# Optimization experiments

Measured on AMD Instinct MI355X. Metric: run time of the kernel, lower is better.

The kernel has to match this reference:

```python
import math
import jax, jax.numpy as jnp
import numpy as np

K = 64            # multiplicity per irrep
NE = 10           # num_elements
N_NODES = 10000
N_EDGES = 100000
AVG_NEIGH = 10.0
EDGE_DIM = 8
LS = [0, 1, 2]    # node/intermediate irreps 64x0e+64x1o+64x2e
LS_OUT = [0, 1]   # output irreps 64x0e+64x1o
INV_SQRT_K = 1.0 / math.sqrt(K)
MIX_NORM = 1.0 / math.sqrt(K * NE)

# ---- real spherical-harmonic Clebsch-Gordan coefficients (small l, exact) ----
def _cg(j1, m1, j2, m2, j3, m3):
    if m1 + m2 != m3 or not (abs(j1 - j2) <= j3 <= j1 + j2):
        return 0.0
    f = math.factorial
    pre = math.sqrt((2 * j3 + 1) * f(j1 + j2 - j3) * f(j1 - j2 + j3) * f(-j1 + j2 + j3) / f(j1 + j2 + j3 + 1))
    pre *= math.sqrt(f(j1 + m1) * f(j1 - m1) * f(j2 + m2) * f(j2 - m2) * f(j3 + m3) * f(j3 - m3))
    s = 0.0
    for k in range(j1 + j2 + j3 + 1):
        d = (j1 + j2 - j3 - k, j1 - m1 - k, j2 + m2 - k, j3 - j2 + m1 + k, j3 - j1 - m2 + k)
        if min(d) < 0:
            continue
        s += (-1) ** k / (f(k) * f(d[0]) * f(d[1]) * f(d[2]) * f(d[3]) * f(d[4]))
    return pre * s

def _u_real(l):
    # complex->real SH change of basis: Y_real = U @ Y_complex
    U = np.zeros((2 * l + 1, 2 * l + 1), dtype=np.complex128)
    U[l, l] = 1.0
    s = 1.0 / math.sqrt(2.0)
    for m in range(1, l + 1):
        U[l + m, l + m] = (-1) ** m * s
        U[l + m, l - m] = s
        U[l - m, l + m] = -1j * (-1) ** m * s
        U[l - m, l - m] = 1j * s
    return U

def real_cg(l1, l2, l3):
    C = np.zeros((2 * l1 + 1, 2 * l2 + 1, 2 * l3 + 1), dtype=np.complex128)
    for m1 in range(-l1, l1 + 1):
        for m2 in range(-l2, l2 + 1):
            m3 = m1 + m2
            if abs(m3) <= l3:
                C[l1 + m1, l2 + m2, l3 + m3] = _cg(l1, m1, l2, m2, l3, m3)
    U1, U2, U3 = _u_real(l1), _u_real(l2), _u_real(l3)
    Cr = np.einsum('ai,bj,ck,ijk->abc', U1, U2, U3.conj(), C)
    return np.ascontiguousarray(Cr.real).astype(np.float32)  # real since l1+l2+l3 even

# parity/triangle allowed paths (l1: edge sph, l2: node in, l3: intermediate) -> 11 paths
EDGE_PATHS = [(l1, l2, l3) for l1 in LS for l2 in LS for l3 in LS
              if abs(l1 - l2) <= l3 <= l1 + l2 and (l1 + l2 + l3) % 2 == 0]
N_EDGE_PATHS = len(EDGE_PATHS)  # 11
DEG2_PATHS = [(0, 0, 0), (1, 1, 0), (2, 2, 0), (0, 1, 1), (1, 2, 1)]
DEG3_PATHS = [(0, 0, 0), (1, 1, 0), (0, 1, 1), (1, 0, 1), (1, 2, 1)]
CG_EDGE = [real_cg(*p) for p in EDGE_PATHS]
CG_D2 = [real_cg(*p) for p in DEG2_PATHS]
CG_D3 = [real_cg(*p) for p in DEG3_PATHS]

def split_irreps(x, ls, mul):
    # ir_mul layout: per irrep a [(2l+1)*mul] flat segment, m index outer
    out, o = [], 0
    for l in ls:
        d = (2 * l + 1) * mul
        out.append(x[:, o:o + d].reshape(x.shape[0], 2 * l + 1, mul))
        o += d
    return out


def setup_inputs() -> dict:
    key = jax.random.key(0)
    ks = jax.random.split(key, 20)
    sender = jax.random.randint(ks[0], (N_EDGES,), 0, N_NODES)
    receiver = jax.random.randint(ks[1], (N_EDGES,), 0, N_NODES)
    indices = jax.random.randint(ks[2], (N_NODES,), 0, NE)
    node_attrs = jax.nn.one_hot(indices, NE, dtype=jnp.float32)
    node_feature_in = jax.random.normal(ks[3], (N_NODES, K * 9), dtype=jnp.float32)
    edge_length_embed = jax.random.normal(ks[4], (N_EDGES, EDGE_DIM), dtype=jnp.float32)
    edge_sph_embed = jax.random.normal(ks[5], (N_EDGES, 9), dtype=jnp.float32)
    W_lin_in = jax.random.normal(ks[6], (3, K, K), dtype=jnp.float32)
    mlp_W0 = jax.random.normal(ks[7], (EDGE_DIM, 32), dtype=jnp.float32) / math.sqrt(EDGE_DIM)
    mlp_b0 = jnp.zeros((32,), jnp.float32)
    mlp_W1 = jax.random.normal(ks[8], (32, 32), dtype=jnp.float32) / math.sqrt(32.0)
    mlp_b1 = jnp.zeros((32,), jnp.float32)
    mlp_W2 = jax.random.normal(ks[9], (32, 32), dtype=jnp.float32) / math.sqrt(32.0)
    mlp_b2 = jnp.zeros((32,), jnp.float32)
    mlp_W3 = jax.random.normal(ks[10], (32, N_EDGE_PATHS * K), dtype=jnp.float32) / math.sqrt(32.0)
    mlp_b3 = jnp.zeros((N_EDGE_PATHS * K,), jnp.float32)
    W_mix = jax.random.normal(ks[11], (3, NE, K, K), dtype=jnp.float32)
    w1 = jax.random.normal(ks[12], (NE, 2, K), dtype=jnp.float32)
    w2 = 0.1 * jax.random.normal(ks[13], (NE, len(DEG2_PATHS), K), dtype=jnp.float32)
    w3 = 0.05 * jax.random.normal(ks[14], (NE, len(DEG3_PATHS), K), dtype=jnp.float32)
    W_out_m = jax.random.normal(ks[15], (2, K, K), dtype=jnp.float32)
    W_out_h = jax.random.normal(ks[16], (2, K, K), dtype=jnp.float32)
    return dict(sender=sender, receiver=receiver, indices=indices, node_attrs=node_attrs,
                node_feature_in=node_feature_in, edge_length_embed=edge_length_embed,
                edge_sph_embed=edge_sph_embed, W_lin_in=W_lin_in,
                mlp_W0=mlp_W0, mlp_b0=mlp_b0, mlp_W1=mlp_W1, mlp_b1=mlp_b1,
                mlp_W2=mlp_W2, mlp_b2=mlp_b2, mlp_W3=mlp_W3, mlp_b3=mlp_b3,
                W_mix=W_mix, w1=w1, w2=w2, w3=w3, W_out_m=W_out_m, W_out_h=W_out_h)


def reference(sender, receiver, indices, node_attrs, node_feature_in,
              edge_length_embed, edge_sph_embed, W_lin_in,
              mlp_W0, mlp_b0, mlp_W1, mlp_b1, mlp_W2, mlp_b2, mlp_W3, mlp_b3,
              W_mix, w1, w2, w3, W_out_m, W_out_h):
    N = node_feature_in.shape[0]
    h1 = split_irreps(node_feature_in, LS, K)  # per-l [N, 2l+1, K]
    # ELinear_h1_2_h1p: per-irrep channel mixing
    h1p = [jnp.einsum('nmc,cd->nmd', h1[l], W_lin_in[l]) * INV_SQRT_K for l in LS]
    # residual radial MLP -> per-edge TP path weights [E, P, K]
    h = jax.nn.silu(edge_length_embed @ mlp_W0 + mlp_b0)
    h = h + jax.nn.silu(h @ mlp_W1 + mlp_b1)
    h = h + jax.nn.silu(h @ mlp_W2 + mlp_b2)
    Rl = (h @ mlp_W3 + mlp_b3).reshape(-1, N_EDGE_PATHS, K)
    sph = split_irreps(edge_sph_embed, LS, 1)  # per-l [E, 2l+1, 1]
    gx = [h1p[l][sender] for l in LS]          # gather sender node features
    # channelwise equivariant tensor product with per-edge radial weights
    msg = [None, None, None]
    for p, (l1, l2, l3) in enumerate(EDGE_PATHS):
        t = jnp.einsum('abd,ea,ebc->edc', jnp.asarray(CG_EDGE[p]), sph[l1][:, :, 0], gx[l2])
        t = t * Rl[:, p, None, :]
        msg[l3] = t if msg[l3] is None else msg[l3] + t
    # scatter-sum messages to receivers, normalized by avg num neighbors
    A = [jax.ops.segment_sum(msg[l], receiver, num_segments=N) / AVG_NEIGH for l in LS]
    # element-conditioned mixing (FCTP with num_elements x 0e attrs)
    Amix = [jnp.einsum('nmc,ne,ecd->nmd', A[l], node_attrs, W_mix[l]) * MIX_NORM for l in LS]
    # symmetric contraction (body order 3) with element-dependent channelwise weights
    w1n, w2n, w3n = w1[indices], w2[indices], w3[indices]
    T2 = [jnp.zeros_like(Amix[L]) for L in LS_OUT]
    for p, (l1, l2, L) in enumerate(DEG2_PATHS):
        t = jnp.einsum('abd,nac,nbc->ndc', jnp.asarray(CG_D2[p]), Amix[l1], Amix[l2])
        T2[L] = T2[L] + w2n[:, p, None, :] * t
    T3 = [jnp.zeros_like(Amix[L]) for L in LS_OUT]
    for q, (Lp, l3, L) in enumerate(DEG3_PATHS):
        t = jnp.einsum('abd,nac,nbc->ndc', jnp.asarray(CG_D3[q]), T2[Lp], Amix[l3])
        T3[L] = T3[L] + w3n[:, q, None, :] * t
    B = [w1n[:, L, None, :] * Amix[L] + T2[L] + T3[L] for L in LS_OUT]
    # node_feature_out = ELinear_h1_2_h2(h1) + ELinear_m2_2_h2(B)
    out = []
    for L in LS_OUT:
        y = jnp.einsum('nmc,cd->nmd', h1[L], W_out_h[L]) * INV_SQRT_K
        y = y + jnp.einsum('nmc,cd->nmd', B[L], W_out_m[L]) * INV_SQRT_K
        out.append(y.reshape(N, -1))
    return jnp.concatenate(out, axis=1)  # [N, 4K] = [N, 256]
```

## Files before the change

### kernel.cpp

```cpp
#include <hip/hip_runtime.h>
#include <math.h>

#define NNODES 10000
#define NEDGES 100000
#define EPW 8

struct Cplx { double re, im; };

constexpr double cfact(int n){ double r=1.0; for(int i=2;i<=n;++i) r*=i; return r; }

constexpr double csqrt_(double x){
  if (x<=0.0) return 0.0;
  double g = x<1.0 ? 1.0 : x;
  for (int it=0; it<64; ++it){ double ng = 0.5*(g + x/g); if (ng==g) break; g = ng; }
  return g;
}

constexpr double cg_coeff(int j1,int m1,int j2,int m2,int j3,int m3){
  if (m1+m2!=m3) return 0.0;
  int lo = j1>j2 ? j1-j2 : j2-j1;
  if (j3<lo || j3>j1+j2) return 0.0;
  if (m1<-j1||m1>j1||m2<-j2||m2>j2||m3<-j3||m3>j3) return 0.0;
  double pre = csqrt_((2.0*j3+1.0)*cfact(j1+j2-j3)*cfact(j1-j2+j3)*cfact(-j1+j2+j3)/cfact(j1+j2+j3+1));
  pre *= csqrt_(cfact(j1+m1)*cfact(j1-m1)*cfact(j2+m2)*cfact(j2-m2)*cfact(j3+m3)*cfact(j3-m3));
  double s = 0.0;
  for (int k=0;k<=j1+j2+j3;++k){
    int d0=j1+j2-j3-k, d1=j1-m1-k, d2=j2+m2-k, d3=j3-j2+m1+k, d4=j3-j1-m2+k;
    if (d0<0||d1<0||d2<0||d3<0||d4<0) continue;
    double term = 1.0/(cfact(k)*cfact(d0)*cfact(d1)*cfact(d2)*cfact(d3)*cfact(d4));
    s += (k&1) ? -term : term;
  }
  return pre*s;
}

constexpr Cplx uent(int l,int a,int i){
  const double s = 0.70710678118654752440;
  int ma = a - l;
  if (ma==0) { if (i==l) return Cplx{1.0,0.0}; return Cplx{0.0,0.0}; }
  if (ma>0){
    int m = ma; double sg = (m&1) ? -1.0 : 1.0;
    if (i==l+m) return Cplx{sg*s, 0.0};
    if (i==l-m) return Cplx{s, 0.0};
    return Cplx{0.0,0.0};
  }
  int m = -ma; double sg = (m&1) ? -1.0 : 1.0;
  if (i==l+m) return Cplx{0.0, -sg*s};
  if (i==l-m) return Cplx{0.0, s};
  return Cplx{0.0,0.0};
}

constexpr double real_cg_entry(int l1,int l2,int l3,int a,int b,int c){
  double acc = 0.0;
  int ii0 = a, ii1 = 2*l1-a;
  int jj0 = b, jj1 = 2*l2-b;
  for (int x=0;x<2;++x){
    int i = (x==0)? ii0 : ii1;
    if (x==1 && ii1==ii0) break;
    Cplx u1 = uent(l1,a,i); if (u1.re==0.0 && u1.im==0.0) continue;
    for (int y=0;y<2;++y){
      int j = (y==0)? jj0 : jj1;
      if (y==1 && jj1==jj0) break;
      Cplx u2 = uent(l2,b,j); if (u2.re==0.0 && u2.im==0.0) continue;
      int k = (i-l1)+(j-l2)+l3;
      if (k<0 || k>2*l3) continue;
      Cplx u3 = uent(l3,c,k); if (u3.re==0.0 && u3.im==0.0) continue;
      double cg = cg_coeff(l1,i-l1,l2,j-l2,l3,k-l3);
      if (cg==0.0) continue;
      double pr = u1.re*u2.re - u1.im*u2.im;
      double pi = u1.re*u2.im + u1.im*u2.re;
      acc += (pr*u3.re + pi*u3.im) * cg;
    }
  }
  return acc;
}

struct CGT { float v[5][5][5]; };
constexpr CGT make_cg(int l1,int l2,int l3){
  CGT t{};
  for (int a=0;a<2*l1+1;++a)
    for (int b=0;b<2*l2+1;++b)
      for (int c=0;c<2*l3+1;++c)
        t.v[a][b][c] = (float)real_cg_entry(l1,l2,l3,a,b,c);
  return t;
}

__device__ __forceinline__ float rdlane(float v, int l){
  return __int_as_float(__builtin_amdgcn_readlane(__float_as_int(v), l));
}
__device__ __forceinline__ float silu_(float x){ return x / (1.0f + __expf(-x)); }

template<int L1,int L2,int L3>
__device__ __forceinline__ void tp_accum(const float* sp, const float* g, float rl, float* msg){
  constexpr CGT T = make_cg(L1,L2,L3);
  constexpr int NA = 2*L1+1, NB = 2*L2+1, ND = 2*L3+1;
  float t[ND];
#pragma unroll
  for (int d=0; d<ND; ++d) t[d] = 0.f;
#pragma unroll
  for (int b=0;b<NB;++b){
#pragma unroll
    for (int d=0; d<ND; ++d){
      float u = 0.f; bool any = false;
#pragma unroll
      for (int a=0;a<NA;++a){
        const float cg = T.v[a][b][d];
        if (cg != 0.f){ u = fmaf(cg, sp[a], u); any = true; }
      }
      if (any) t[d] = fmaf(u, g[b], t[d]);
    }
  }
#pragma unroll
  for (int d=0;d<ND;++d) msg[d] = fmaf(rl, t[d], msg[d]);
}

template<int L1,int L2,int L3>
__device__ __forceinline__ void sc_accum(const float* X, const float* Y, float w, float* out){
  constexpr CGT T = make_cg(L1,L2,L3);
  constexpr int NA = 2*L1+1, NB = 2*L2+1, ND = 2*L3+1;
#pragma unroll
  for (int d=0;d<ND;++d){
    float s = 0.f;
#pragma unroll
    for (int a=0;a<NA;++a){
#pragma unroll
      for (int b=0;b<NB;++b){
        const float cg = T.v[a][b][d];
        if (cg != 0.f) s = fmaf(cg*X[a], Y[b], s);
      }
    }
    out[d] = fmaf(w, s, out[d]);
  }
}

__global__ void __launch_bounds__(64) k_lin_in(const float* __restrict__ h1,
                                               const float* __restrict__ W,
                                               float* __restrict__ h1p){
  const int n = blockIdx.x;
  const int d = threadIdx.x;
  const float* row = h1 + (long)n*576;
  float acc[9];
#pragma unroll
  for (int i=0;i<9;++i) acc[i] = 0.f;
  for (int c=0;c<64;++c){
    const float w0 = W[c*64 + d];
    const float w1 = W[4096 + c*64 + d];
    const float w2 = W[8192 + c*64 + d];
    acc[0] = fmaf(row[c], w0, acc[0]);
#pragma unroll
    for (int m=0;m<3;++m) acc[1+m] = fmaf(row[64+m*64+c], w1, acc[1+m]);
#pragma unroll
    for (int m=0;m<5;++m) acc[4+m] = fmaf(row[256+m*64+c], w2, acc[4+m]);
  }
  float* o = h1p + (long)n*576;
  o[d] = acc[0]*0.125f;
#pragma unroll
  for (int m=0;m<3;++m) o[64+m*64+d] = acc[1+m]*0.125f;
#pragma unroll
  for (int m=0;m<5;++m) o[256+m*64+d] = acc[4+m]*0.125f;
}

__global__ void __launch_bounds__(64) k_edge(const int* __restrict__ sender,
                                             const int* __restrict__ receiver,
                                             const float* __restrict__ ele,
                                             const float* __restrict__ sph,
                                             const float* __restrict__ h1p,
                                             const float* __restrict__ W0, const float* __restrict__ b0,
                                             const float* __restrict__ W1, const float* __restrict__ b1,
                                             const float* __restrict__ W2, const float* __restrict__ b2,
                                             const float* __restrict__ W3, const float* __restrict__ b3,
                                             float* __restrict__ A){
  const int lane = threadIdx.x;
  const int j32 = lane & 31;
  const long base = (long)blockIdx.x * EPW;

  float h[EPW];
#pragma unroll
  for (int e8=0;e8<EPW;++e8){
    const float* xr = ele + (base+e8)*8;
    float acc = b0[j32];
#pragma unroll
    for (int i=0;i<8;++i) acc = fmaf(xr[i], W0[i*32+j32], acc);
    h[e8] = silu_(acc);
  }
#pragma unroll
  for (int L=0; L<2; ++L){
    const float* Wl = L ? W2 : W1;
    const float* bl = L ? b2 : b1;
    float acc[EPW];
#pragma unroll
    for (int e8=0;e8<EPW;++e8) acc[e8] = bl[j32];
    for (int j=0;j<32;++j){
      const float w = Wl[j*32+j32];
#pragma unroll
      for (int e8=0;e8<EPW;++e8) acc[e8] = fmaf(rdlane(h[e8], j), w, acc[e8]);
    }
#pragma unroll
    for (int e8=0;e8<EPW;++e8) h[e8] += silu_(acc[e8]);
  }
  float rl[EPW][11];
#pragma unroll
  for (int e8=0;e8<EPW;++e8)
#pragma unroll
    for (int p=0;p<11;++p) rl[e8][p] = b3[p*64+lane];
  for (int j=0;j<32;++j){
    float w3v[11];
#pragma unroll
    for (int p=0;p<11;++p) w3v[p] = W3[j*704 + p*64 + lane];
#pragma unroll
    for (int e8=0;e8<EPW;++e8){
      const float hj = rdlane(h[e8], j);
#pragma unroll
      for (int p=0;p<11;++p) rl[e8][p] = fmaf(hj, w3v[p], rl[e8][p]);
    }
  }

#pragma unroll
  for (int e8=0;e8<EPW;++e8){
    const long e = base + e8;
    const int s = sender[e];
    const int r = receiver[e];
    const float* sp = sph + e*9;
    float spv[9];
#pragma unroll
    for (int i=0;i<9;++i) spv[i] = sp[i];
    const float* hp = h1p + (long)s*576;
    float g0[1], g1[3], g2[5];
    g0[0] = hp[lane];
#pragma unroll
    for (int m=0;m<3;++m) g1[m] = hp[64+m*64+lane];
#pragma unroll
    for (int m=0;m<5;++m) g2[m] = hp[256+m*64+lane];
    float m0[1] = {0.f};
    float m1[3] = {0.f,0.f,0.f};
    float m2[5] = {0.f,0.f,0.f,0.f,0.f};
    tp_accum<0,0,0>(spv+0, g0, rl[e8][0],  m0);
    tp_accum<0,1,1>(spv+0, g1, rl[e8][1],  m1);
    tp_accum<0,2,2>(spv+0, g2, rl[e8][2],  m2);
    tp_accum<1,0,1>(spv+1, g0, rl[e8][3],  m1);
    tp_accum<1,1,0>(spv+1, g1, rl[e8][4],  m0);
    tp_accum<1,1,2>(spv+1, g1, rl[e8][5],  m2);
    tp_accum<1,2,1>(spv+1, g2, rl[e8][6],  m1);
    tp_accum<2,0,2>(spv+4, g0, rl[e8][7],  m2);
    tp_accum<2,1,1>(spv+4, g1, rl[e8][8],  m1);
    tp_accum<2,2,0>(spv+4, g2, rl[e8][9],  m0);
    tp_accum<2,2,2>(spv+4, g2, rl[e8][10], m2);
    float* Ar = A + (long)r*576;
    atomicAdd(&Ar[lane], m0[0]);
#pragma unroll
    for (int m=0;m<3;++m) atomicAdd(&Ar[64+m*64+lane], m1[m]);
#pragma unroll
    for (int m=0;m<5;++m) atomicAdd(&Ar[256+m*64+lane], m2[m]);
  }
}

__global__ void __launch_bounds__(64) k_node(const int* __restrict__ indices,
                                             const float* __restrict__ h1,
                                             const float* __restrict__ A,
                                             const float* __restrict__ Wmix,
                                             const float* __restrict__ w1,
                                             const float* __restrict__ w2,
                                             const float* __restrict__ w3,
                                             const float* __restrict__ Wom,
                                             const float* __restrict__ Woh,
                                             float* __restrict__ out){
  __shared__ float Bsh[4][64];
  const int n = blockIdx.x;
  const int lane = threadIdx.x;
  const int e = indices[n];
  const float* Ar = A + (long)n*576;
  float ax[9];
#pragma unroll
  for (int i=0;i<9;++i) ax[i] = 0.f;
  {
    const float* Wm0 = Wmix + (size_t)(0*10 + e)*4096;
    const float* Wm1 = Wmix + (size_t)(1*10 + e)*4096;
    const float* Wm2 = Wmix + (size_t)(2*10 + e)*4096;
    for (int c=0;c<64;++c){
      const float wv0 = Wm0[c*64+lane];
      const float wv1 = Wm1[c*64+lane];
      const float wv2 = Wm2[c*64+lane];
      ax[0] = fmaf(Ar[c], wv0, ax[0]);
#pragma unroll
      for (int m=0;m<3;++m) ax[1+m] = fmaf(Ar[64+m*64+c], wv1, ax[1+m]);
#pragma unroll
      for (int m=0;m<5;++m) ax[4+m] = fmaf(Ar[256+m*64+c], wv2, ax[4+m]);
    }
  }
#pragma unroll
  for (int i=0;i<9;++i) ax[i] *= 0.0039528470752104741f;

  const float* amix0 = ax;
  const float* amix1 = ax+1;
  const float* amix2 = ax+4;
  float w2n[5], w3n[5];
#pragma unroll
  for (int p=0;p<5;++p){
    w2n[p] = w2[(size_t)(e*5+p)*64 + lane];
    w3n[p] = w3[(size_t)(e*5+p)*64 + lane];
  }
  float t20[1] = {0.f}, t21[3] = {0.f,0.f,0.f};
  sc_accum<0,0,0>(amix0, amix0, w2n[0], t20);
  sc_accum<1,1,0>(amix1, amix1, w2n[1], t20);
  sc_accum<2,2,0>(amix2, amix2, w2n[2], t20);
  sc_accum<0,1,1>(amix0, amix1, w2n[3], t21);
  sc_accum<1,2,1>(amix1, amix2, w2n[4], t21);
  float t30[1] = {0.f}, t31[3] = {0.f,0.f,0.f};
  sc_accum<0,0,0>(t20, amix0, w3n[0], t30);
  sc_accum<1,1,0>(t21, amix1, w3n[1], t30);
  sc_accum<0,1,1>(t20, amix1, w3n[2], t31);
  sc_accum<1,0,1>(t21, amix0, w3n[3], t31);
  sc_accum<1,2,1>(t21, amix2, w3n[4], t31);

  const float w1_0 = w1[(size_t)(e*2+0)*64 + lane];
  const float w1_1 = w1[(size_t)(e*2+1)*64 + lane];
  Bsh[0][lane] = fmaf(w1_0, amix0[0], t20[0] + t30[0]);
#pragma unroll
  for (int m=0;m<3;++m) Bsh[1+m][lane] = fmaf(w1_1, amix1[m], t21[m] + t31[m]);
  __syncthreads();

  const float* hrow = h1 + (long)n*576;
  float o[4];
#pragma unroll
  for (int i=0;i<4;++i) o[i] = 0.f;
  for (int c=0;c<64;++c){
    const float wh0 = Woh[c*64+lane];
    const float wh1 = Woh[4096 + c*64+lane];
    const float wm0 = Wom[c*64+lane];
    const float wm1 = Wom[4096 + c*64+lane];
    o[0] = fmaf(hrow[c], wh0, o[0]);
    o[0] = fmaf(Bsh[0][c], wm0, o[0]);
#pragma unroll
    for (int m=0;m<3;++m){
      o[1+m] = fmaf(hrow[64+m*64+c], wh1, o[1+m]);
      o[1+m] = fmaf(Bsh[1+m][c], wm1, o[1+m]);
    }
  }
  float* orow = out + (long)n*256;
  orow[lane] = o[0]*0.125f;
#pragma unroll
  for (int m=0;m<3;++m) orow[64+m*64+lane] = o[1+m]*0.125f;
}

extern "C" void kernel_launch(void* const* d_in, const int* in_sizes, int n_in,
                              void* d_out, int out_size, void* d_ws, size_t ws_size,
                              hipStream_t stream){
  const int*   sender   = (const int*)  d_in[0];
  const int*   receiver = (const int*)  d_in[1];
  const int*   indices  = (const int*)  d_in[2];
  const float* node_feat= (const float*)d_in[4];
  const float* ele      = (const float*)d_in[5];
  const float* sph      = (const float*)d_in[6];
  const float* W_lin    = (const float*)d_in[7];
  const float* W0 = (const float*)d_in[8],  *b0 = (const float*)d_in[9];
  const float* W1 = (const float*)d_in[10], *b1 = (const float*)d_in[11];
  const float* W2 = (const float*)d_in[12], *b2 = (const float*)d_in[13];
  const float* W3 = (const float*)d_in[14], *b3 = (const float*)d_in[15];
  const float* Wmix = (const float*)d_in[16];
  const float* w1 = (const float*)d_in[17];
  const float* w2 = (const float*)d_in[18];
  const float* w3 = (const float*)d_in[19];
  const float* Wom = (const float*)d_in[20];
  const float* Woh = (const float*)d_in[21];
  float* out = (float*)d_out;

  float* h1p = (float*)d_ws;
  float* A   = h1p + (size_t)NNODES*576;

  hipMemsetAsync(A, 0, (size_t)NNODES*576*sizeof(float), stream);
  k_lin_in<<<NNODES, 64, 0, stream>>>(node_feat, W_lin, h1p);
  k_edge<<<NEDGES/EPW, 64, 0, stream>>>(sender, receiver, ele, sph, h1p,
                                        W0,b0,W1,b1,W2,b2,W3,b3, A);
  k_node<<<NNODES, 64, 0, stream>>>(indices, node_feat, A, Wmix, w1, w2, w3, Wom, Woh, out);
}
```

Baseline: 305.8 us.

## Split edge kernel by output irrep to cut registers, fuse A zeroing into linear

The edge kernel's radial-weight computation and tensor-product stage are split into three phases, one per output irrep (l=0, 1, 2). Each phase keeps only 3-4 radial weights per edge live instead of all 11, which lowers register pressure. The cost is re-gathering the sender features three times and recomputing the rdlane broadcasts. The kernel also packs four waves per 256-thread block, stages the spherical harmonics in shared memory, and zeroes A inside k_lin_in instead of a separate memset.

```diff
diff --git a/kernel.cpp b/kernel.cpp
--- a/kernel.cpp
+++ b/kernel.cpp
@@ -134,9 +134,13 @@
 
 __global__ void __launch_bounds__(64) k_lin_in(const float* __restrict__ h1,
                                                const float* __restrict__ W,
-                                               float* __restrict__ h1p){
+                                               float* __restrict__ h1p,
+                                               float* __restrict__ A){
   const int n = blockIdx.x;
   const int d = threadIdx.x;
+  float* Az = A + (long)n*576;
+#pragma unroll
+  for (int i=0;i<9;++i) Az[i*64+d] = 0.f;
   const float* row = h1 + (long)n*576;
   float acc[9];
 #pragma unroll
@@ -159,7 +163,7 @@
   for (int m=0;m<5;++m) o[256+m*64+d] = acc[4+m]*0.125f;
 }
 
-__global__ void __launch_bounds__(64) k_edge(const int* __restrict__ sender,
+__global__ void __launch_bounds__(256) k_edge(const int* __restrict__ sender,
                                              const int* __restrict__ receiver,
                                              const float* __restrict__ ele,
                                              const float* __restrict__ sph,
@@ -169,18 +173,23 @@
                                              const float* __restrict__ W2, const float* __restrict__ b2,
                                              const float* __restrict__ W3, const float* __restrict__ b3,
                                              float* __restrict__ A){
-  const int lane = threadIdx.x;
-  const int j32 = lane & 31;
-  const long base = (long)blockIdx.x * EPW;
+  __shared__ float sps[4][EPW*9];
+  const int wid  = threadIdx.x >> 6;
+  const int lane = threadIdx.x & 63;
+  const int j32  = lane & 31;
+  const long base = ((long)blockIdx.x*4 + wid) * EPW;
+
+  sps[wid][lane < EPW*9 ? lane : 0] = sph[base*9 + (lane < EPW*9 ? lane : 0)];
+  if (lane < EPW*9 - 64) sps[wid][64+lane] = sph[base*9 + 64 + lane];
 
   float h[EPW];
 #pragma unroll
-  for (int e8=0;e8<EPW;++e8){
-    const float* xr = ele + (base+e8)*8;
+  for (int e=0;e<EPW;++e){
+    const float* xr = ele + (base+e)*8;
     float acc = b0[j32];
 #pragma unroll
     for (int i=0;i<8;++i) acc = fmaf(xr[i], W0[i*32+j32], acc);
-    h[e8] = silu_(acc);
+    h[e] = silu_(acc);
   }
 #pragma unroll
   for (int L=0; L<2; ++L){
@@ -188,68 +197,139 @@
     const float* bl = L ? b2 : b1;
     float acc[EPW];
 #pragma unroll
-    for (int e8=0;e8<EPW;++e8) acc[e8] = bl[j32];
+    for (int e=0;e<EPW;++e) acc[e] = bl[j32];
     for (int j=0;j<32;++j){
       const float w = Wl[j*32+j32];
 #pragma unroll
-      for (int e8=0;e8<EPW;++e8) acc[e8] = fmaf(rdlane(h[e8], j), w, acc[e8]);
-    }
-#pragma unroll
-    for (int e8=0;e8<EPW;++e8) h[e8] += silu_(acc[e8]);
-  }
-  float rl[EPW][11];
-#pragma unroll
-  for (int e8=0;e8<EPW;++e8)
-#pragma unroll
-    for (int p=0;p<11;++p) rl[e8][p] = b3[p*64+lane];
-  for (int j=0;j<32;++j){
-    float w3v[11];
-#pragma unroll
-    for (int p=0;p<11;++p) w3v[p] = W3[j*704 + p*64 + lane];
-#pragma unroll
-    for (int e8=0;e8<EPW;++e8){
-      const float hj = rdlane(h[e8], j);
-#pragma unroll
-      for (int p=0;p<11;++p) rl[e8][p] = fmaf(hj, w3v[p], rl[e8][p]);
-    }
-  }
-
-#pragma unroll
-  for (int e8=0;e8<EPW;++e8){
-    const long e = base + e8;
-    const int s = sender[e];
-    const int r = receiver[e];
-    const float* sp = sph + e*9;
-    float spv[9];
-#pragma unroll
-    for (int i=0;i<9;++i) spv[i] = sp[i];
-    const float* hp = h1p + (long)s*576;
-    float g0[1], g1[3], g2[5];
-    g0[0] = hp[lane];
-#pragma unroll
-    for (int m=0;m<3;++m) g1[m] = hp[64+m*64+lane];
-#pragma unroll
-    for (int m=0;m<5;++m) g2[m] = hp[256+m*64+lane];
-    float m0[1] = {0.f};
-    float m1[3] = {0.f,0.f,0.f};
-    float m2[5] = {0.f,0.f,0.f,0.f,0.f};
-    tp_accum<0,0,0>(spv+0, g0, rl[e8][0],  m0);
-    tp_accum<0,1,1>(spv+0, g1, rl[e8][1],  m1);
-    tp_accum<0,2,2>(spv+0, g2, rl[e8][2],  m2);
-    tp_accum<1,0,1>(spv+1, g0, rl[e8][3],  m1);
-    tp_accum<1,1,0>(spv+1, g1, rl[e8][4],  m0);
-    tp_accum<1,1,2>(spv+1, g1, rl[e8][5],  m2);
-    tp_accum<1,2,1>(spv+1, g2, rl[e8][6],  m1);
-    tp_accum<2,0,2>(spv+4, g0, rl[e8][7],  m2);
-    tp_accum<2,1,1>(spv+4, g1, rl[e8][8],  m1);
-    tp_accum<2,2,0>(spv+4, g2, rl[e8][9],  m0);
-    tp_accum<2,2,2>(spv+4, g2, rl[e8][10], m2);
-    float* Ar = A + (long)r*576;
-    atomicAdd(&Ar[lane], m0[0]);
-#pragma unroll
-    for (int m=0;m<3;++m) atomicAdd(&Ar[64+m*64+lane], m1[m]);
-#pragma unroll
-    for (int m=0;m<5;++m) atomicAdd(&Ar[256+m*64+lane], m2[m]);
+      for (int e=0;e<EPW;++e) acc[e] = fmaf(rdlane(h[e], j), w, acc[e]);
+    }
+#pragma unroll
+    for (int e=0;e<EPW;++e) h[e] += silu_(acc[e]);
+  }
+
+  {
+    float rl[3][EPW];
+    {
+      const float bb0 = b3[0*64+lane], bb4 = b3[4*64+lane], bb9 = b3[9*64+lane];
+#pragma unroll
+      for (int e=0;e<EPW;++e){ rl[0][e]=bb0; rl[1][e]=bb4; rl[2][e]=bb9; }
+    }
+    for (int j=0;j<32;++j){
+      const float w_0 = W3[j*704 + 0*64 + lane];
+      const float w_4 = W3[j*704 + 4*64 + lane];
+      const float w_9 = W3[j*704 + 9*64 + lane];
+#pragma unroll
+      for (int e=0;e<EPW;++e){
+        const float hj = rdlane(h[e], j);
+        rl[0][e] = fmaf(hj, w_0, rl[0][e]);
+        rl[1][e] = fmaf(hj, w_4, rl[1][e]);
+        rl[2][e] = fmaf(hj, w_9, rl[2][e]);
+      }
+    }
+#pragma unroll
+    for (int e=0;e<EPW;++e){
+      const int s = sender[base+e];
+      const float* hp = h1p + (long)s*576;
+      float g0[1], g1[3], g2[5];
+      g0[0] = hp[lane];
+#pragma unroll
+      for (int m=0;m<3;++m) g1[m] = hp[64+m*64+lane];
+#pragma unroll
+      for (int m=0;m<5;++m) g2[m] = hp[256+m*64+lane];
+      const float* sp = &sps[wid][e*9];
+      float m0[1] = {0.f};
+      tp_accum<0,0,0>(sp+0, g0, rl[0][e], m0);
+      tp_accum<1,1,0>(sp+1, g1, rl[1][e], m0);
+      tp_accum<2,2,0>(sp+4, g2, rl[2][e], m0);
+      const int r = receiver[base+e];
+      atomicAdd(&A[(long)r*576 + lane], m0[0]);
+    }
+  }
+
+  {
+    float rl[4][EPW];
+    {
+      const float bb1 = b3[1*64+lane], bb3 = b3[3*64+lane], bb6 = b3[6*64+lane], bb8 = b3[8*64+lane];
+#pragma unroll
+      for (int e=0;e<EPW;++e){ rl[0][e]=bb1; rl[1][e]=bb3; rl[2][e]=bb6; rl[3][e]=bb8; }
+    }
+    for (int j=0;j<32;++j){
+      const float w_1 = W3[j*704 + 1*64 + lane];
+      const float w_3 = W3[j*704 + 3*64 + lane];
+      const float w_6 = W3[j*704 + 6*64 + lane];
+      const float w_8 = W3[j*704 + 8*64 + lane];
+#pragma unroll
+      for (int e=0;e<EPW;++e){
+        const float hj = rdlane(h[e], j);
+        rl[0][e] = fmaf(hj, w_1, rl[0][e]);
+        rl[1][e] = fmaf(hj, w_3, rl[1][e]);
+        rl[2][e] = fmaf(hj, w_6, rl[2][e]);
+        rl[3][e] = fmaf(hj, w_8, rl[3][e]);
+      }
+    }
+#pragma unroll
+    for (int e=0;e<EPW;++e){
+      const int s = sender[base+e];
+      const float* hp = h1p + (long)s*576;
+      float g0[1], g1[3], g2[5];
+      g0[0] = hp[lane];
+#pragma unroll
+      for (int m=0;m<3;++m) g1[m] = hp[64+m*64+lane];
+#pragma unroll
+      for (int m=0;m<5;++m) g2[m] = hp[256+m*64+lane];
+      const float* sp = &sps[wid][e*9];
+      float m1[3] = {0.f,0.f,0.f};
+      tp_accum<0,1,1>(sp+0, g1, rl[0][e], m1);
+      tp_accum<1,0,1>(sp+1, g0, rl[1][e], m1);
+      tp_accum<1,2,1>(sp+1, g2, rl[2][e], m1);
+      tp_accum<2,1,1>(sp+4, g1, rl[3][e], m1);
+      const int r = receiver[base+e];
+#pragma unroll
+      for (int m=0;m<3;++m) atomicAdd(&A[(long)r*576 + 64 + m*64 + lane], m1[m]);
+    }
+  }
+
+  {
+    float rl[4][EPW];
+    {
+      const float bb2 = b3[2*64+lane], bb5 = b3[5*64+lane], bb7 = b3[7*64+lane], bb10 = b3[10*64+lane];
+#pragma unroll
+      for (int e=0;e<EPW;++e){ rl[0][e]=bb2; rl[1][e]=bb5; rl[2][e]=bb7; rl[3][e]=bb10; }
+    }
+    for (int j=0;j<32;++j){
+      const float w_2  = W3[j*704 + 2*64 + lane];
+      const float w_5  = W3[j*704 + 5*64 + lane];
+      const float w_7  = W3[j*704 + 7*64 + lane];
+      const float w_10 = W3[j*704 + 10*64 + lane];
+#pragma unroll
+      for (int e=0;e<EPW;++e){
+        const float hj = rdlane(h[e], j);
+        rl[0][e] = fmaf(hj, w_2,  rl[0][e]);
+        rl[1][e] = fmaf(hj, w_5,  rl[1][e]);
+        rl[2][e] = fmaf(hj, w_7,  rl[2][e]);
+        rl[3][e] = fmaf(hj, w_10, rl[3][e]);
+      }
+    }
+#pragma unroll
+    for (int e=0;e<EPW;++e){
+      const int s = sender[base+e];
+      const float* hp = h1p + (long)s*576;
+      float g0[1], g1[3], g2[5];
+      g0[0] = hp[lane];
+#pragma unroll
+      for (int m=0;m<3;++m) g1[m] = hp[64+m*64+lane];
+#pragma unroll
+      for (int m=0;m<5;++m) g2[m] = hp[256+m*64+lane];
+      const float* sp = &sps[wid][e*9];
+      float m2[5] = {0.f,0.f,0.f,0.f,0.f};
+      tp_accum<0,2,2>(sp+0, g2, rl[0][e], m2);
+      tp_accum<1,1,2>(sp+1, g1, rl[1][e], m2);
+      tp_accum<2,0,2>(sp+4, g0, rl[2][e], m2);
+      tp_accum<2,2,2>(sp+4, g2, rl[3][e], m2);
+      const int r = receiver[base+e];
+#pragma unroll
+      for (int m=0;m<5;++m) atomicAdd(&A[(long)r*576 + 256 + m*64 + lane], m2[m]);
+    }
   }
 }
 
@@ -366,9 +446,8 @@
   float* h1p = (float*)d_ws;
   float* A   = h1p + (size_t)NNODES*576;
 
-  hipMemsetAsync(A, 0, (size_t)NNODES*576*sizeof(float), stream);
-  k_lin_in<<<NNODES, 64, 0, stream>>>(node_feat, W_lin, h1p);
-  k_edge<<<NEDGES/EPW, 64, 0, stream>>>(sender, receiver, ele, sph, h1p,
-                                        W0,b0,W1,b1,W2,b2,W3,b3, A);
+  k_lin_in<<<NNODES, 64, 0, stream>>>(node_feat, W_lin, h1p, A);
+  k_edge<<<NEDGES/(4*EPW), 256, 0, stream>>>(sender, receiver, ele, sph, h1p,
+                                             W0,b0,W1,b1,W2,b2,W3,b3, A);
   k_node<<<NNODES, 64, 0, stream>>>(indices, node_feat, A, Wmix, w1, w2, w3, Wom, Woh, out);
 }
```

After: 310.1 us. Within noise of the previous version (+1.4%).
